# Kernel tuning notes

Measured on AMD Instinct MI355X. Metric: run time of the kernel, lower is better.

The kernel has to match this reference:

```python
import math
import jax, jax.numpy as jnp
import numpy as np

SCALING = 16.0 / 32.0  # alpha / rank


def real_fourier_orthogonal_multiply(c):
    """Vectorized equivalent of the per-frequency Python loop: build a complex
    spectrum from real Fourier coefficients and inverse-rfft along last dim."""
    n = c.shape[-1]
    sqrt_n = math.sqrt(n)
    pair_scale = math.sqrt(n / 2.0)
    max_f = (n - 1) // 2
    work = c.astype(jnp.float32)
    dc = (work[..., 0] * sqrt_n)[..., None].astype(jnp.complex64)
    cos = work[..., 1:1 + 2 * max_f:2] * pair_scale
    sin = work[..., 2:2 + 2 * max_f:2] * pair_scale
    mid = (cos - 1j * sin).astype(jnp.complex64)  # freqs 1..max_f
    parts = [dc, mid]
    if n % 2 == 0:
        parts.append((work[..., -1] * sqrt_n)[..., None].astype(jnp.complex64))
    spectrum = jnp.concatenate(parts, axis=-1)  # [..., n//2+1]
    return jnp.fft.irfft(spectrum, n=n, axis=-1).astype(c.dtype)


def setup_inputs() -> dict:
    key = jax.random.key(0)
    ks = jax.random.split(key, 9)
    B, S, D_in, D_out, R0, R1, E = 4, 2048, 4096, 4096, 32, 8, 3
    x = jax.random.normal(ks[0], (B, S, D_in), dtype=jnp.float32)
    W_base = jax.random.normal(ks[1], (D_out, D_in), dtype=jnp.float32) * 0.02
    b_base = jax.random.normal(ks[2], (D_out,), dtype=jnp.float32) * 0.02
    enc0 = jax.random.normal(ks[3], (R0, D_in), dtype=jnp.float32) * 0.02
    enc1 = jax.random.normal(ks[4], (R1, D_in), dtype=jnp.float32) * 0.02
    coefs0 = jax.random.normal(ks[5], (E, D_out, R0), dtype=jnp.float32) * 0.02
    coefs1 = jax.random.normal(ks[6], (E, D_out, R1), dtype=jnp.float32) * 0.02
    # sparse decoder masks (buffers in the torch module)
    mask0 = jax.random.randint(ks[7], (E, D_out, R0), 0, 2).astype(bool)
    mask1 = jax.random.randint(ks[8], (E, D_out, R1), 0, 2).astype(bool)
    return dict(x=x, W_base=W_base, b_base=b_base, enc0=enc0, enc1=enc1,
                coefs0=coefs0, coefs1=coefs1, mask0=mask0, mask1=mask1)


def reference(x, W_base, b_base, enc0, enc1, coefs0, coefs1, mask0, mask1):
    # base linear
    base = jnp.einsum('bsd,od->bso', x, W_base) + b_base
    # encoder blocks (shared across experts)
    e0 = jnp.einsum('bsd,rd->bsr', x, enc0)  # [B,S,R0]
    e1 = jnp.einsum('bsd,rd->bsr', x, enc1)  # [B,S,R1]
    # masked decoder blocks per expert, summed over blocks
    w0 = coefs0 * mask0.astype(coefs0.dtype)  # [E,O,R0]
    w1 = coefs1 * mask1.astype(coefs1.dtype)  # [E,O,R1]
    decoded = (jnp.einsum('bsr,eor->ebso', e0, w0)
               + jnp.einsum('bsr,eor->ebso', e1, w1))  # [E,B,S,O]
    transformed = real_fourier_orthogonal_multiply(decoded)
    update = transformed.sum(axis=0)  # sum over active experts
    return base + update * SCALING
```

## Files before the change

### kernel.cpp

```cpp
#include <hip/hip_runtime.h>

typedef __attribute__((ext_vector_type(2))) float f32x2;
typedef __attribute__((ext_vector_type(4))) float f32x4;
typedef __attribute__((ext_vector_type(16))) float f32x16;
typedef __attribute__((ext_vector_type(8))) short bf16x8;
typedef __attribute__((ext_vector_type(8))) unsigned short u16x8;

#define GL2LDS(g, l) __builtin_amdgcn_global_load_lds( \
    (const __attribute__((address_space(1))) void*)(g), \
    (__attribute__((address_space(3))) void*)(l), 16, 0, 0)

__device__ __forceinline__ unsigned short f2bf(float x) {
    union { float f; unsigned u; } v; v.f = x;
    unsigned r = (v.u + 0x7FFF + ((v.u >> 16) & 1)) >> 16;
    return (unsigned short)r;
}

__global__ __launch_bounds__(256) void k_prep(const float* __restrict__ c0,
                                              const float* __restrict__ c1,
                                              const int* __restrict__ m0,
                                              const int* __restrict__ m1,
                                              float* __restrict__ Wc,
                                              const float* __restrict__ x,
                                              unsigned short* __restrict__ xb) {
    int b = blockIdx.x;
    if (b < 640) {
        int idx = b * 256 + threadIdx.x;
        if (idx >= 4096 * 40) return;
        int o = idx / 40, c = idx % 40;
        float s = 0.f;
        if (c < 32) {
            #pragma unroll
            for (int e = 0; e < 3; ++e) {
                int i = (e * 4096 + o) * 32 + c;
                s += c0[i] * (m0[i] != 0 ? 1.f : 0.f);
            }
        } else {
            int r = c - 32;
            #pragma unroll
            for (int e = 0; e < 3; ++e) {
                int i = (e * 4096 + o) * 8 + r;
                s += c1[i] * (m1[i] != 0 ? 1.f : 0.f);
            }
        }
        Wc[idx] = s;
    } else {
        int idx = (b - 640) * 256 + threadIdx.x;
        f32x4 f0 = ((const f32x4*)x)[(size_t)idx * 2];
        f32x4 f1 = ((const f32x4*)x)[(size_t)idx * 2 + 1];
        u16x8 o;
        o[0] = f2bf(f0[0]); o[1] = f2bf(f0[1]); o[2] = f2bf(f0[2]); o[3] = f2bf(f0[3]);
        o[4] = f2bf(f1[0]); o[5] = f2bf(f1[1]); o[6] = f2bf(f1[2]); o[7] = f2bf(f1[3]);
        *(u16x8*)(xb + (size_t)idx * 8) = o;
    }
}

__global__ __launch_bounds__(256) void k_gmat(const float* __restrict__ Wc,
                                              float* __restrict__ G) {
    __shared__ float lds[10752];
    int tid = threadIdx.x;
    int t_base = blockIdx.x * 8;
    int f_slot = tid & 31;
    int tg = (tid >> 5) & 1;
    int rg = tid >> 6;
    float acc[4][10];
    #pragma unroll
    for (int a = 0; a < 4; ++a)
        #pragma unroll
        for (int b = 0; b < 10; ++b) acc[a][b] = 0.f;

    for (int ch = 0; ch < 16; ++ch) {
        __syncthreads();
        #pragma unroll
        for (int j = 0; j < 10; ++j) {
            int idx = tid + j * 256;
            int row = idx / 20;
            int v = idx % 20;
            int f = ch * 128 + row;
            f32x4 val = {0.f, 0.f, 0.f, 0.f};
            if (f >= 1) val = *(const f32x4*)(Wc + (2 * f - 1) * 40 + v * 4);
            *(f32x4*)(lds + row * 84 + v * 4) = val;
        }
        __syncthreads();
        #pragma unroll
        for (int j2 = 0; j2 < 4; ++j2) {
            int f_local = f_slot + 32 * j2;
            int f = ch * 128 + f_local;
            float cs[4], sn[4];
            #pragma unroll
            for (int tt = 0; tt < 4; ++tt) {
                int t = t_base + tg * 4 + tt;
                int ph = (f * t) & 4095;
                float rev = (float)ph * (1.0f / 4096.0f);
                cs[tt] = __builtin_amdgcn_cosf(rev);
                sn[tt] = __builtin_amdgcn_sinf(rev);
            }
            const float* Lc = lds + f_local * 84 + rg * 10;
            const float* Ls = Lc + 40;
            #pragma unroll
            for (int rr = 0; rr < 10; ++rr) {
                float wc = Lc[rr], ws = Ls[rr];
                #pragma unroll
                for (int tt = 0; tt < 4; ++tt)
                    acc[tt][rr] += cs[tt] * wc + sn[tt] * ws;
            }
        }
    }
    __syncthreads();
    #pragma unroll
    for (int tt = 0; tt < 4; ++tt)
        #pragma unroll
        for (int rr = 0; rr < 10; ++rr)
            lds[tid * 40 + tt * 10 + rr] = acc[tt][rr];
    __syncthreads();
    for (int oi = tid; oi < 320; oi += 256) {
        int t_local = oi / 40, rc = oi % 40;
        int tg2 = t_local >> 2, tsub = t_local & 3;
        int rg2 = rc / 10, rsub = rc % 10;
        float s = 0.f;
        #pragma unroll
        for (int fs = 0; fs < 32; ++fs)
            s += lds[(fs + tg2 * 32 + rg2 * 64) * 40 + tsub * 10 + rsub];
        int t = t_base + t_local;
        float dc = Wc[rc];
        float ny = Wc[4095 * 40 + rc];
        float sign = (t & 1) ? -1.f : 1.f;
        float g = 0.5f * (0.0220970869120796f * s + (dc + sign * ny) * (1.0f / 64.0f));
        G[t * 40 + rc] = g;
    }
}

__global__ __launch_bounds__(256) void k_wcomb(const float* __restrict__ Wb,
                                               const float* __restrict__ enc0,
                                               const float* __restrict__ enc1,
                                               const float* __restrict__ G,
                                               unsigned short* __restrict__ Wcb) {
    __shared__ float ldsE[40 * 256];
    __shared__ float ldsG[32 * 40];
    int tid = threadIdx.x;
    int d0 = blockIdx.x * 256;
    int t0 = blockIdx.y * 32;
    #pragma unroll
    for (int j = 0; j < 10; ++j) {
        int idx = tid + j * 256;
        int k = idx / 64, v = idx % 64;
        const float* src = (k < 32) ? (enc0 + (size_t)k * 4096) : (enc1 + (size_t)(k - 32) * 4096);
        *(f32x4*)(ldsE + k * 256 + v * 4) = *(const f32x4*)(src + d0 + v * 4);
    }
    #pragma unroll
    for (int j = 0; j < 5; ++j) {
        int idx = tid + j * 256;
        ldsG[idx] = G[(size_t)(t0 + idx / 40) * 40 + (idx % 40)];
    }
    __syncthreads();
    int dg = tid & 31, tg = tid >> 5;
    f32x2 a[4][4];
    #pragma unroll
    for (int s = 0; s < 4; ++s)
        #pragma unroll
        for (int tt = 0; tt < 4; ++tt) a[s][tt] = (f32x2){0.f, 0.f};
    #pragma unroll 8
    for (int r = 0; r < 40; ++r) {
        f32x2 e[4];
        #pragma unroll
        for (int s = 0; s < 4; ++s)
            e[s] = *(const f32x2*)(ldsE + r * 256 + s * 64 + dg * 2);
        #pragma unroll
        for (int tt = 0; tt < 4; ++tt) {
            float g = ldsG[(tg * 4 + tt) * 40 + r];
            #pragma unroll
            for (int s = 0; s < 4; ++s)
                a[s][tt] += g * e[s];
        }
    }
    #pragma unroll
    for (int tt = 0; tt < 4; ++tt) {
        int t = t0 + tg * 4 + tt;
        #pragma unroll
        for (int s = 0; s < 4; ++s) {
            int d = d0 + s * 64 + dg * 2;
            f32x2 wv = *(const f32x2*)(Wb + (size_t)t * 4096 + d);
            f32x2 rv = a[s][tt] + wv;
            unsigned short lo = f2bf(rv[0]), hi = f2bf(rv[1]);
            *(unsigned*)(Wcb + (size_t)t * 4096 + d) = (unsigned)lo | ((unsigned)hi << 16);
        }
    }
}

__global__ __launch_bounds__(512, 2) void k_gemm(const unsigned short* __restrict__ A,
                                                 const unsigned short* __restrict__ B,
                                                 const float* __restrict__ bias,
                                                 float* __restrict__ C) {
    __shared__ __align__(16) short As[2][256 * 64];
    __shared__ __align__(16) short Bs[2][256 * 64];
    const int tid = threadIdx.x;
    const int lane = tid & 63, w = tid >> 6;
    const int wm = w >> 2, wn = w & 3;
    const int l15 = lane & 15;
    const int kc = lane >> 4;
    const int sk = lane & 7;

    int bid = blockIdx.x;
    int swz = (bid & 7) * 64 + (bid >> 3);
    int m0 = (swz >> 4) * 256;
    int n0 = (swz & 15) * 256;

    const int srow = w * 8 + (lane >> 3);
    const int scg  = (lane & 7) ^ ((lane >> 3) & 7);
    const unsigned short* Ag = A + (size_t)(m0 + srow) * 4096 + scg * 8;
    const unsigned short* Bg = B + (size_t)(n0 + srow) * 4096 + scg * 8;

#define STAGE(buf, kt) do { \
    _Pragma("unroll") \
    for (int c = 0; c < 4; ++c) { \
        GL2LDS(Ag + (size_t)(c * 64) * 4096 + (kt), &As[buf][(c * 64 + w * 8) * 64]); \
        GL2LDS(Bg + (size_t)(c * 64) * 4096 + (kt), &Bs[buf][(c * 64 + w * 8) * 64]); \
    } \
} while (0)

    int aoff[8], boff[4];
    #pragma unroll
    for (int mt = 0; mt < 8; ++mt) aoff[mt] = (wm * 128 + mt * 16 + l15) * 64;
    #pragma unroll
    for (int nt = 0; nt < 4; ++nt) boff[nt] = (wn * 64 + nt * 16 + l15) * 64;
    const int s0 = ((0 + kc) ^ sk) * 8;
    const int s1 = ((4 + kc) ^ sk) * 8;

    f32x4 acc[8][4];
    #pragma unroll
    for (int mt = 0; mt < 8; ++mt)
        #pragma unroll
        for (int nt = 0; nt < 4; ++nt)
            #pragma unroll
            for (int r = 0; r < 4; ++r) acc[mt][nt][r] = 0.f;

#define TILE_BODY(CB, kt, DO_STAGE, WAITK) do { \
    bf16x8 aF[8][2], bF[4][2]; \
    _Pragma("unroll") \
    for (int mt = 0; mt < 8; ++mt) { \
        aF[mt][0] = *(const bf16x8*)&As[CB][aoff[mt] + s0]; \
        aF[mt][1] = *(const bf16x8*)&As[CB][aoff[mt] + s1]; \
    } \
    _Pragma("unroll") \
    for (int nt = 0; nt < 4; ++nt) { \
        bF[nt][0] = *(const bf16x8*)&Bs[CB][boff[nt] + s0]; \
        bF[nt][1] = *(const bf16x8*)&Bs[CB][boff[nt] + s1]; \
    } \
    __builtin_amdgcn_s_setprio(1); \
    _Pragma("unroll") \
    for (int kh = 0; kh < 2; ++kh) \
        _Pragma("unroll") \
        for (int mt = 0; mt < 8; ++mt) \
            _Pragma("unroll") \
            for (int nt = 0; nt < 2; ++nt) \
                acc[mt][nt] = __builtin_amdgcn_mfma_f32_16x16x32_bf16(aF[mt][kh], bF[nt][kh], acc[mt][nt], 0, 0, 0); \
    __builtin_amdgcn_s_setprio(0); \
    asm volatile("s_barrier" ::: "memory"); \
    if (DO_STAGE) STAGE(CB, (kt) + 128); \
    __builtin_amdgcn_s_setprio(1); \
    _Pragma("unroll") \
    for (int kh = 0; kh < 2; ++kh) \
        _Pragma("unroll") \
        for (int mt = 0; mt < 8; ++mt) \
            _Pragma("unroll") \
            for (int nt = 2; nt < 4; ++nt) \
                acc[mt][nt] = __builtin_amdgcn_mfma_f32_16x16x32_bf16(aF[mt][kh], bF[nt][kh], acc[mt][nt], 0, 0, 0); \
    __builtin_amdgcn_s_setprio(0); \
    if ((WAITK) == 8) { \
        asm volatile("s_waitcnt vmcnt(8)\n\ts_barrier" ::: "memory"); \
    } else if ((WAITK) == 0) { \
        asm volatile("s_waitcnt vmcnt(0)\n\ts_barrier" ::: "memory"); \
    } \
} while (0)

    STAGE(0, 0);
    STAGE(1, 64);
    asm volatile("s_waitcnt vmcnt(8)\n\ts_barrier" ::: "memory");

    for (int i = 0; i < 31; ++i) {
        int kt = i * 128;
        TILE_BODY(0, kt, true, 8);
        TILE_BODY(1, kt + 64, true, 8);
    }
    TILE_BODY(0, 62 * 64, false, 0);
    TILE_BODY(1, 63 * 64, false, -1);
#undef TILE_BODY
#undef STAGE

    const int r4 = (lane >> 4) * 4;
    float bv[4];
    #pragma unroll
    for (int nt = 0; nt < 4; ++nt) bv[nt] = bias[n0 + wn * 64 + nt * 16 + l15];
    #pragma unroll
    for (int mt = 0; mt < 8; ++mt) {
        #pragma unroll
        for (int nt = 0; nt < 4; ++nt) {
            #pragma unroll
            for (int r = 0; r < 4; ++r) {
                int row = m0 + wm * 128 + mt * 16 + r4 + r;
                C[(size_t)row * 4096 + n0 + wn * 64 + nt * 16 + l15] = acc[mt][nt][r] + bv[nt];
            }
        }
    }
}

extern "C" void kernel_launch(void* const* d_in, const int* in_sizes, int n_in,
                              void* d_out, int out_size, void* d_ws, size_t ws_size,
                              hipStream_t stream) {
    const float* x   = (const float*)d_in[0];
    const float* Wb  = (const float*)d_in[1];
    const float* bb  = (const float*)d_in[2];
    const float* e0  = (const float*)d_in[3];
    const float* e1  = (const float*)d_in[4];
    const float* c0  = (const float*)d_in[5];
    const float* c1  = (const float*)d_in[6];
    const int*   m0  = (const int*)d_in[7];
    const int*   m1  = (const int*)d_in[8];
    float* out = (float*)d_out;

    char* ws = (char*)d_ws;
    unsigned short* xb  = (unsigned short*)ws;
    float* Wc           = (float*)(ws + 67108864);
    float* G            = (float*)(ws + 67764224);
    unsigned short* Wcb = (unsigned short*)(ws + 68419584);

    k_prep <<<17024, 256, 0, stream>>>(c0, c1, m0, m1, Wc, x, xb);
    k_gmat <<<512, 256, 0, stream>>>(Wc, G);
    k_wcomb<<<dim3(16, 128), 256, 0, stream>>>(Wb, e0, e1, G, Wcb);
    k_gemm <<<512, 512, 0, stream>>>(xb, Wcb, bb, out);
}
```

Before: 592.7 us.

## Interleave LDS fragment reads, MFMA quadrants and staged global loads in GEMM

Restructures the bf16 GEMM main loop into an 8-phase window. Each K tile is split into four MFMA quadrants, and each quadrant is preceded by partial LDS fragment reads and one chunk of global-to-LDS staging. This replaces the earlier approach of loading whole tiles and then running two MFMA halves. The aim is finer-grained overlap of LDS reads, global loads and matrix math, in the style of a ping-pong schedule. In exchange it adds many more barriers and waitcnts per tile, which could serialize the waves and slow the loop.

```diff
diff --git a/kernel.cpp b/kernel.cpp
--- a/kernel.cpp
+++ b/kernel.cpp
@@ -210,12 +210,9 @@
     const unsigned short* Ag = A + (size_t)(m0 + srow) * 4096 + scg * 8;
     const unsigned short* Bg = B + (size_t)(n0 + srow) * 4096 + scg * 8;
 
-#define STAGE(buf, kt) do { \
-    _Pragma("unroll") \
-    for (int c = 0; c < 4; ++c) { \
-        GL2LDS(Ag + (size_t)(c * 64) * 4096 + (kt), &As[buf][(c * 64 + w * 8) * 64]); \
-        GL2LDS(Bg + (size_t)(c * 64) * 4096 + (kt), &Bs[buf][(c * 64 + w * 8) * 64]); \
-    } \
+#define SU(buf, kt, u) do { \
+    GL2LDS(Ag + (size_t)((u) * 64) * 4096 + (kt), &As[buf][((u) * 64 + w * 8) * 64]); \
+    GL2LDS(Bg + (size_t)((u) * 64) * 4096 + (kt), &Bs[buf][((u) * 64 + w * 8) * 64]); \
 } while (0)
 
     int aoff[8], boff[4];
@@ -234,58 +231,86 @@
             #pragma unroll
             for (int r = 0; r < 4; ++r) acc[mt][nt][r] = 0.f;
 
-#define TILE_BODY(CB, kt, DO_STAGE, WAITK) do { \
-    bf16x8 aF[8][2], bF[4][2]; \
+    bf16x8 aF[8][2], bF[4][2];
+
+#define RD12(CB) do { \
+    bF[0][0] = *(const bf16x8*)&Bs[CB][boff[0] + s0]; \
+    bF[1][0] = *(const bf16x8*)&Bs[CB][boff[1] + s0]; \
+    bF[0][1] = *(const bf16x8*)&Bs[CB][boff[0] + s1]; \
+    bF[1][1] = *(const bf16x8*)&Bs[CB][boff[1] + s1]; \
     _Pragma("unroll") \
-    for (int mt = 0; mt < 8; ++mt) { \
+    for (int mt = 0; mt < 4; ++mt) { \
         aF[mt][0] = *(const bf16x8*)&As[CB][aoff[mt] + s0]; \
         aF[mt][1] = *(const bf16x8*)&As[CB][aoff[mt] + s1]; \
     } \
+} while (0)
+#define RD8(CB) do { \
     _Pragma("unroll") \
-    for (int nt = 0; nt < 4; ++nt) { \
-        bF[nt][0] = *(const bf16x8*)&Bs[CB][boff[nt] + s0]; \
-        bF[nt][1] = *(const bf16x8*)&Bs[CB][boff[nt] + s1]; \
+    for (int mt = 4; mt < 8; ++mt) { \
+        aF[mt][0] = *(const bf16x8*)&As[CB][aoff[mt] + s0]; \
+        aF[mt][1] = *(const bf16x8*)&As[CB][aoff[mt] + s1]; \
     } \
-    __builtin_amdgcn_s_setprio(1); \
+} while (0)
+#define RD4(CB) do { \
+    bF[2][0] = *(const bf16x8*)&Bs[CB][boff[2] + s0]; \
+    bF[3][0] = *(const bf16x8*)&Bs[CB][boff[3] + s0]; \
+    bF[2][1] = *(const bf16x8*)&Bs[CB][boff[2] + s1]; \
+    bF[3][1] = *(const bf16x8*)&Bs[CB][boff[3] + s1]; \
+} while (0)
+
+#define MQ(MB, NB) do { \
     _Pragma("unroll") \
     for (int kh = 0; kh < 2; ++kh) \
         _Pragma("unroll") \
-        for (int mt = 0; mt < 8; ++mt) \
+        for (int mt = 0; mt < 4; ++mt) \
             _Pragma("unroll") \
             for (int nt = 0; nt < 2; ++nt) \
-                acc[mt][nt] = __builtin_amdgcn_mfma_f32_16x16x32_bf16(aF[mt][kh], bF[nt][kh], acc[mt][nt], 0, 0, 0); \
-    __builtin_amdgcn_s_setprio(0); \
-    asm volatile("s_barrier" ::: "memory"); \
-    if (DO_STAGE) STAGE(CB, (kt) + 128); \
-    __builtin_amdgcn_s_setprio(1); \
-    _Pragma("unroll") \
-    for (int kh = 0; kh < 2; ++kh) \
-        _Pragma("unroll") \
-        for (int mt = 0; mt < 8; ++mt) \
-            _Pragma("unroll") \
-            for (int nt = 2; nt < 4; ++nt) \
-                acc[mt][nt] = __builtin_amdgcn_mfma_f32_16x16x32_bf16(aF[mt][kh], bF[nt][kh], acc[mt][nt], 0, 0, 0); \
-    __builtin_amdgcn_s_setprio(0); \
-    if ((WAITK) == 8) { \
-        asm volatile("s_waitcnt vmcnt(8)\n\ts_barrier" ::: "memory"); \
-    } else if ((WAITK) == 0) { \
-        asm volatile("s_waitcnt vmcnt(0)\n\ts_barrier" ::: "memory"); \
-    } \
-} while (0)
-
-    STAGE(0, 0);
-    STAGE(1, 64);
-    asm volatile("s_waitcnt vmcnt(8)\n\ts_barrier" ::: "memory");
-
-    for (int i = 0; i < 31; ++i) {
-        int kt = i * 128;
-        TILE_BODY(0, kt, true, 8);
-        TILE_BODY(1, kt + 64, true, 8);
-    }
-    TILE_BODY(0, 62 * 64, false, 0);
-    TILE_BODY(1, 63 * 64, false, -1);
-#undef TILE_BODY
-#undef STAGE
+                acc[MB + mt][NB + nt] = __builtin_amdgcn_mfma_f32_16x16x32_bf16( \
+                    aF[MB + mt][kh], bF[NB + nt][kh], acc[MB + mt][NB + nt], 0, 0, 0); \
+} while (0)
+
+#define BAR       __builtin_amdgcn_s_barrier()
+#define LGKM0     asm volatile("s_waitcnt lgkmcnt(0)" ::: "memory")
+#define LGKM8     asm volatile("s_waitcnt lgkmcnt(8)" ::: "memory")
+#define VM2BAR    asm volatile("s_waitcnt vmcnt(2)\n\ts_barrier" ::: "memory")
+#define VM0BAR    asm volatile("s_waitcnt vmcnt(0)\n\ts_barrier" ::: "memory")
+#define PRIO(x)   __builtin_amdgcn_s_setprio(x)
+
+#define WINDOW(DOA, DOB, DOC, W3, W7, KT) do { \
+     RD12(0); if (DOA) SU(1, (KT) + 64, 1); LGKM8; \
+              BAR; LGKM0; PRIO(1); MQ(0, 0); PRIO(0); BAR; \
+     RD8(0);  if (DOA) SU(1, (KT) + 64, 2); \
+              BAR; LGKM0; PRIO(1); MQ(4, 0); PRIO(0); BAR; \
+     RD4(0);  if (DOA) SU(1, (KT) + 64, 3); \
+              BAR; LGKM0; PRIO(1); MQ(4, 2); PRIO(0); BAR; \
+              if (DOB) SU(0, (KT) + 128, 0); \
+              BAR; LGKM0; PRIO(1); MQ(0, 2); PRIO(0); \
+              if ((W3) == 2) { VM2BAR; } else { VM0BAR; } \
+     RD12(1); if (DOB) SU(0, (KT) + 128, 1); LGKM8; \
+              BAR; LGKM0; PRIO(1); MQ(0, 0); PRIO(0); BAR; \
+     RD8(1);  if (DOB) SU(0, (KT) + 128, 2); \
+              BAR; LGKM0; PRIO(1); MQ(4, 0); PRIO(0); BAR; \
+     RD4(1);  if (DOB) SU(0, (KT) + 128, 3); \
+              BAR; LGKM0; PRIO(1); MQ(4, 2); PRIO(0); BAR; \
+              if (DOC) SU(1, (KT) + 192, 0); \
+              BAR; LGKM0; PRIO(1); MQ(0, 2); PRIO(0); \
+              if ((W7) == 2) { VM2BAR; } \
+} while (0)
+
+    SU(0, 0, 0); SU(0, 0, 1); SU(0, 0, 2); SU(0, 0, 3);
+    SU(1, 64, 0);
+    VM2BAR;
+
+    for (int j = 0; j < 31; ++j)
+        WINDOW(true, true, true, 2, 2, j * 128);
+    WINDOW(true, false, false, 0, -1, 31 * 128);
+
+#undef WINDOW
+#undef SU
+#undef RD12
+#undef RD8
+#undef RD4
+#undef MQ
 
     const int r4 = (lane >> 4) * 4;
     float bv[4];
```

New measurement: 637.5 us. +7.6%, slower.
